# Kernel tuning notes

Hardware: AMD Instinct MI355X
Metric: run time of the kernel (lower is better)

## Reference

```python
import jax, jax.numpy as jnp
import numpy as np

D = 768
HEAD_SIZE = 64  # D / num_heads = 768 / 12

def setup_inputs() -> dict:
    key = jax.random.key(0)
    k1, k2, k3, k4 = jax.random.split(key, 4)
    ix = jax.random.normal(k1, (8, 4096, D), dtype=jnp.float32)
    # Linear(D, head_size, bias=False) weights; stored as [D, head_size] for x @ W
    scale = 1.0 / np.sqrt(D)
    Wk = jax.random.uniform(k2, (D, HEAD_SIZE), dtype=jnp.float32, minval=-scale, maxval=scale)
    Wq = jax.random.uniform(k3, (D, HEAD_SIZE), dtype=jnp.float32, minval=-scale, maxval=scale)
    Wv = jax.random.uniform(k4, (D, HEAD_SIZE), dtype=jnp.float32, minval=-scale, maxval=scale)
    return {"ix": ix, "Wk": Wk, "Wq": Wq, "Wv": Wv}

def reference(ix, Wk, Wq, Wv):
    # ix: [B, S, D]
    k = ix @ Wk  # [B, S, H]
    q = ix @ Wq  # [B, S, H]
    v = ix @ Wv  # [B, S, H]
    scale = 1.0 / jnp.sqrt(jnp.asarray(HEAD_SIZE, ix.dtype))
    wei = jnp.einsum('bsh,bth->bst', q, k) * scale  # [B, S, S]
    wei = jax.nn.softmax(wei, axis=-1)
    out = jnp.einsum('bst,bth->bsh', wei, v)  # [B, S, H]
    return out
```

## Files before the change

kernel.cpp:

```cpp
#include <hip/hip_runtime.h>
#include <hip/hip_bf16.h>

#define D_DIM 768
#define HS 64
#define SEQ 4096
#define NBATCH 8

typedef short bf8 __attribute__((ext_vector_type(8)));
typedef short bf4 __attribute__((ext_vector_type(4)));
typedef float f4 __attribute__((ext_vector_type(4)));

static __device__ __forceinline__ short f2b(float x) {
    __hip_bfloat16 h = __float2bfloat16(x);
    return __builtin_bit_cast(short, h);
}
static __device__ __forceinline__ unsigned pk2(float x, float y) {
    unsigned ux = __builtin_bit_cast(unsigned, x) + 0x8000u;
    unsigned uy = __builtin_bit_cast(unsigned, y) + 0x8000u;
    return __builtin_amdgcn_perm(uy, ux, 0x07060302u);
}

#if defined(__has_builtin)
#if __has_builtin(__builtin_amdgcn_exp2f)
#define EXP2F(x) __builtin_amdgcn_exp2f(x)
#endif
#endif
#ifndef EXP2F
#define EXP2F(x) exp2f(x)
#endif

__global__ __launch_bounds__(256) void wconv_kernel(
    const float* __restrict__ Wk, const float* __restrict__ Wq,
    const float* __restrict__ Wv, short* __restrict__ wt3)
{
    int tid = blockIdx.x * 256 + threadIdx.x;
    int mat = tid / (D_DIM * HS);
    int rem = tid - mat * (D_DIM * HS);
    int k = rem >> 6;
    int n = rem & 63;
    const float* W = (mat == 0) ? Wk : (mat == 1) ? Wq : Wv;
    float scale = (mat == 1) ? 0.18033688011112042f : 1.0f;
    int cc = mat * HS + n;
    int c = k >> 5, q = (k >> 3) & 3, e = k & 7;
    wt3[(c * 192 + cc) * 32 + q * 8 + e] = f2b(W[rem] * scale);
}

__global__ __launch_bounds__(256, 3) void proj_kernel(
    const float* __restrict__ ix, const short* __restrict__ wt3,
    short* __restrict__ qg, short* __restrict__ kg, short* __restrict__ vg)
{
    __shared__ short ixl[2][32 * 72];

    const int t = threadIdx.x;
    const int wave = t >> 6, lane = t & 63;
    const int m = lane & 15, quad = lane >> 4;
    const int m0 = blockIdx.x * 32;

    const int srow = t >> 3;
    const int skoff = (t & 7) * 8;

    f4 xr0, xr1;
    auto load_ix = [&](int c) {
        const float* px = ix + (m0 + srow) * D_DIM + c * 64 + skoff;
        xr0 = *(const f4*)px;
        xr1 = *(const f4*)(px + 4);
    };
    auto write_ix = [&](int p) {
        bf8 xw;
        #pragma unroll
        for (int i = 0; i < 4; ++i) { xw[i] = f2b(xr0[i]); xw[i + 4] = f2b(xr1[i]); }
        *(bf8*)(&ixl[p][srow * 72 + skoff]) = xw;
    };

    const int colb = wave * 48;
    const short* wbase = wt3 + (colb + m) * 32 + quad * 8;

    bf8 wb[2][2][3];
    auto load_w = [&](int c, int buf) {
        #pragma unroll
        for (int nt = 0; nt < 3; ++nt) {
            const short* pw = wbase + ((size_t)(2 * c) * 192 + nt * 16) * 32;
            wb[buf][0][nt] = *(const bf8*)pw;
            wb[buf][1][nt] = *(const bf8*)(pw + 192 * 32);
        }
    };

    f4 acc[2][3] = {};

    load_ix(0); load_w(0, 0); write_ix(0); __syncthreads();

    #pragma unroll
    for (int c = 0; c < 12; ++c) {
        const int p = c & 1;
        if (c + 1 < 12) { load_ix(c + 1); load_w(c + 1, (c + 1) & 1); }

        bf8 a0 = *(const bf8*)(&ixl[p][m * 72 + quad * 8]);
        bf8 a1 = *(const bf8*)(&ixl[p][m * 72 + 32 + quad * 8]);
        bf8 a2 = *(const bf8*)(&ixl[p][(16 + m) * 72 + quad * 8]);
        bf8 a3 = *(const bf8*)(&ixl[p][(16 + m) * 72 + 32 + quad * 8]);

        #pragma unroll
        for (int nt = 0; nt < 3; ++nt) {
            acc[0][nt] = __builtin_amdgcn_mfma_f32_16x16x32_bf16(a0, wb[p][0][nt], acc[0][nt], 0, 0, 0);
            acc[0][nt] = __builtin_amdgcn_mfma_f32_16x16x32_bf16(a1, wb[p][1][nt], acc[0][nt], 0, 0, 0);
            acc[1][nt] = __builtin_amdgcn_mfma_f32_16x16x32_bf16(a2, wb[p][0][nt], acc[1][nt], 0, 0, 0);
            acc[1][nt] = __builtin_amdgcn_mfma_f32_16x16x32_bf16(a3, wb[p][1][nt], acc[1][nt], 0, 0, 0);
        }

        if (c + 1 < 12) { write_ix((c + 1) & 1); __syncthreads(); }
    }

    #pragma unroll
    for (int mt = 0; mt < 2; ++mt) {
        const int row = m0 + mt * 16 + quad * 4;
        #pragma unroll
        for (int nt = 0; nt < 3; ++nt) {
            const int cb = colb + nt * 16;
            short* op = (cb < 64) ? kg : (cb < 128) ? qg : vg;
            const int n = (cb & 63) + m;
            #pragma unroll
            for (int r = 0; r < 4; ++r)
                op[(row + r) * HS + n] = f2b(acc[mt][nt][r]);
        }
    }
}

__global__ __launch_bounds__(256, 2) void attn_kernel(
    const short* __restrict__ qg, const short* __restrict__ kg,
    const short* __restrict__ vg, float* __restrict__ num0,
    float* __restrict__ num1, float* __restrict__ num2,
    float* __restrict__ num3, float* __restrict__ den0,
    float* __restrict__ den1, float* __restrict__ den2,
    float* __restrict__ den3)
{
    __shared__ short kl[2][64 * 72];
    __shared__ short vl[2][64 * 64];

    const int t = threadIdx.x;
    const int wave = t >> 6, lane = t & 63;
    const int m = lane & 15, quad = lane >> 4;

    const int flat = blockIdx.x;
    const int lg = (flat & 7) * 64 + (flat >> 3);
    const int qx = lg & 15;
    const int ks = (lg >> 4) & 3;
    const int b  = lg >> 6;

    const int rbase = b * SEQ;
    const int kbase = rbase + ks * (SEQ / 4);
    const int qw = qx * 256 + wave * 64;

    float* __restrict__ nump = (ks == 0) ? num0 : (ks == 1) ? num1 : (ks == 2) ? num2 : num3;
    float* __restrict__ denp = (ks == 0) ? den0 : (ks == 1) ? den1 : (ks == 2) ? den2 : den3;

    bf8 qf[4][2];
    #pragma unroll
    for (int nq = 0; nq < 4; ++nq)
        #pragma unroll
        for (int st = 0; st < 2; ++st)
            qf[nq][st] = *(const bf8*)(qg + (rbase + qw + nq * 16 + m) * HS + st * 32 + quad * 8);

    const int srow = t >> 2, soff = (t & 3) * 16;
    const int jp = t >> 3, dg = t & 7;
    const int j0 = jp * 2;
    const int jj = j0 & 31;
    const int gj = j0 >> 5;
    const int vq = (jj >> 2) & 3;
    const int vh = (jj >> 4) & 1;
    const int vb = (jj & 3) >> 1;
    const int vcol_base = vh * 4 + 2 * vb;
    const int vchunk_l = 4 * gj + vq;

    uint4 kr0, kr1, vr0, vr1;
    auto load_chunk = [&](int c) {
        const short* pk = kg + (kbase + c * 64 + srow) * HS + soff;
        kr0 = *(const uint4*)pk; kr1 = *(const uint4*)(pk + 8);
        const short* pv = vg + (kbase + c * 64 + j0) * HS + dg * 8;
        vr0 = *(const uint4*)pv; vr1 = *(const uint4*)(pv + HS);
    };
    auto write_chunk = [&](int p) {
        *(bf8*)(&kl[p][srow * 72 + soff])     = __builtin_bit_cast(bf8, kr0);
        *(bf8*)(&kl[p][srow * 72 + soff + 8]) = __builtin_bit_cast(bf8, kr1);
        bf8 v0 = __builtin_bit_cast(bf8, vr0), v1 = __builtin_bit_cast(bf8, vr1);
        #pragma unroll
        for (int i = 0; i < 8; ++i) {
            const int d = dg * 8 + i;
            const int chunk = vchunk_l ^ (i ^ dg);
            unsigned val = (unsigned short)v0[i] | ((unsigned)(unsigned short)v1[i] << 16);
            *(unsigned*)(&vl[p][d * 64 + chunk * 8 + vcol_base]) = val;
        }
    };

    f4 o[4][4] = {};
    float den[4] = {0.f, 0.f, 0.f, 0.f};

    load_chunk(0); write_chunk(0); __syncthreads();

    const int NCH = SEQ / 4 / 64;
    for (int c = 0; c < NCH; ++c) {
        const int p = c & 1;
        if (c + 1 < NCH) load_chunk(c + 1);

        #pragma unroll
        for (int g = 0; g < 2; ++g) {
            bf8 kA0 = *(const bf8*)(&kl[p][(g * 32 + m) * 72 + quad * 8]);
            bf8 kA1 = *(const bf8*)(&kl[p][(g * 32 + m) * 72 + 32 + quad * 8]);
            bf8 kB0 = *(const bf8*)(&kl[p][(g * 32 + 16 + m) * 72 + quad * 8]);
            bf8 kB1 = *(const bf8*)(&kl[p][(g * 32 + 16 + m) * 72 + 32 + quad * 8]);

            bf8 vf[4];
            #pragma unroll
            for (int dt = 0; dt < 4; ++dt) {
                const int row = dt * 16 + m;
                const int key = (m & 7) ^ (2 * dt + (m >> 3));
                const int chunk = (g * 4 + quad) ^ key;
                vf[dt] = *(const bf8*)(&vl[p][row * 64 + chunk * 8]);
            }

            #pragma unroll
            for (int nq = 0; nq < 4; ++nq) {
                f4 sa = {0.f, 0.f, 0.f, 0.f}, sb = {0.f, 0.f, 0.f, 0.f};
                sa = __builtin_amdgcn_mfma_f32_16x16x32_bf16(kA0, qf[nq][0], sa, 0, 0, 0);
                sa = __builtin_amdgcn_mfma_f32_16x16x32_bf16(kA1, qf[nq][1], sa, 0, 0, 0);
                sb = __builtin_amdgcn_mfma_f32_16x16x32_bf16(kB0, qf[nq][0], sb, 0, 0, 0);
                sb = __builtin_amdgcn_mfma_f32_16x16x32_bf16(kB1, qf[nq][1], sb, 0, 0, 0);
                float e0 = EXP2F(sa[0]), e1 = EXP2F(sa[1]), e2 = EXP2F(sa[2]), e3 = EXP2F(sa[3]);
                float e4 = EXP2F(sb[0]), e5 = EXP2F(sb[1]), e6 = EXP2F(sb[2]), e7 = EXP2F(sb[3]);
                den[nq] += ((e0 + e1) + (e2 + e3)) + ((e4 + e5) + (e6 + e7));
                uint4 pu;
                pu.x = pk2(e0, e1); pu.y = pk2(e2, e3);
                pu.z = pk2(e4, e5); pu.w = pk2(e6, e7);
                bf8 pf = __builtin_bit_cast(bf8, pu);
                #pragma unroll
                for (int dt = 0; dt < 4; ++dt)
                    o[nq][dt] = __builtin_amdgcn_mfma_f32_16x16x32_bf16(vf[dt], pf, o[nq][dt], 0, 0, 0);
            }
        }

        if (c + 1 < NCH) { write_chunk((c + 1) & 1); __syncthreads(); }
    }

    #pragma unroll
    for (int nq = 0; nq < 4; ++nq) {
        float d = den[nq];
        d += __shfl_xor(d, 16, 64);
        d += __shfl_xor(d, 32, 64);
        const int orow = rbase + qw + nq * 16 + m;
        if (quad == 0) denp[orow] = d;
        #pragma unroll
        for (int dt = 0; dt < 4; ++dt)
            *(f4*)(nump + orow * HS + dt * 16 + quad * 4) = o[nq][dt];
    }
}

__global__ __launch_bounds__(256) void reduce_kernel(
    float* __restrict__ out, const float* __restrict__ num1,
    const float* __restrict__ num2, const float* __restrict__ num3,
    const float* __restrict__ den0, const float* __restrict__ den1,
    const float* __restrict__ den2, const float* __restrict__ den3)
{
    const int gid = blockIdx.x * 256 + threadIdx.x;
    const int base = gid * 4;
    const int r = base >> 6;
    f4 n0 = *(const f4*)(out + base);
    f4 n1 = *(const f4*)(num1 + base);
    f4 n2 = *(const f4*)(num2 + base);
    f4 n3 = *(const f4*)(num3 + base);
    const float rs = 1.0f / ((den0[r] + den1[r]) + (den2[r] + den3[r]));
    f4 res;
    #pragma unroll
    for (int i = 0; i < 4; ++i) res[i] = ((n0[i] + n1[i]) + (n2[i] + n3[i])) * rs;
    *(f4*)(out + base) = res;
}

extern "C" void kernel_launch(void* const* d_in, const int* in_sizes, int n_in,
                              void* d_out, int out_size, void* d_ws, size_t ws_size,
                              hipStream_t stream) {
    const float* ix = (const float*)d_in[0];
    const float* Wk = (const float*)d_in[1];
    const float* Wq = (const float*)d_in[2];
    const float* Wv = (const float*)d_in[3];
    float* out = (float*)d_out;

    const size_t NQKV = (size_t)NBATCH * SEQ * HS;
    short* qg = (short*)d_ws;
    short* kg = qg + NQKV;
    short* vg = kg + NQKV;
    short* wt3 = vg + NQKV;
    char*  fbase = (char*)(wt3 + 24 * 192 * 32);
    float* num1 = (float*)fbase;
    float* num2 = num1 + NQKV;
    float* num3 = num2 + NQKV;
    float* den0 = num3 + NQKV;
    float* den1 = den0 + (size_t)NBATCH * SEQ;
    float* den2 = den1 + (size_t)NBATCH * SEQ;
    float* den3 = den2 + (size_t)NBATCH * SEQ;

    wconv_kernel<<<(3 * D_DIM * HS) / 256, 256, 0, stream>>>(Wk, Wq, Wv, wt3);
    proj_kernel<<<(NBATCH * SEQ) / 32, 256, 0, stream>>>(ix, wt3, qg, kg, vg);
    attn_kernel<<<512, 256, 0, stream>>>(qg, kg, vg, out, num1, num2, num3,
                                         den0, den1, den2, den3);
    reduce_kernel<<<(int)(NQKV / (256 * 4)), 256, 0, stream>>>(
        out, num1, num2, num3, den0, den1, den2, den3);
}
```

Measured before the change: 216.8 us.

## Load K fragments straight from global into registers, restage V, raise proj occupancy

The attention kernel no longer stages K through shared memory. Each wave loads its K MFMA fragments directly from global memory into double-buffered register sets, and the V staging is rewritten to use 4-row ushort4 loads with a new swizzled LDS write. Both kernels' loops are manually unrolled by two so the register buffers can ping-pong, and proj_kernel's launch bounds go from 3 to 4 blocks per CU. This is meant to cut LDS traffic and LDS footprint in attention. In exchange, each wave issues redundant global K loads and register pressure rises, which could cause spills at the higher proj occupancy.

Result: slower. 341.6 us (+57.5%).

```diff
diff --git a/kernel.cpp b/kernel.cpp
--- a/kernel.cpp
+++ b/kernel.cpp
@@ -45,7 +45,7 @@
     wt3[(c * 192 + cc) * 32 + q * 8 + e] = f2b(W[rem] * scale);
 }
 
-__global__ __launch_bounds__(256, 3) void proj_kernel(
+__global__ __launch_bounds__(256, 4) void proj_kernel(
     const float* __restrict__ ix, const short* __restrict__ wt3,
     short* __restrict__ qg, short* __restrict__ kg, short* __restrict__ vg)
 {
@@ -75,39 +75,42 @@
     const int colb = wave * 48;
     const short* wbase = wt3 + (colb + m) * 32 + quad * 8;
 
-    bf8 wb[2][2][3];
-    auto load_w = [&](int c, int buf) {
+    bf8 wbA[2][3], wbB[2][3];
+    auto load_w = [&](int c, bf8 (&dst)[2][3]) {
         #pragma unroll
         for (int nt = 0; nt < 3; ++nt) {
             const short* pw = wbase + ((size_t)(2 * c) * 192 + nt * 16) * 32;
-            wb[buf][0][nt] = *(const bf8*)pw;
-            wb[buf][1][nt] = *(const bf8*)(pw + 192 * 32);
+            dst[0][nt] = *(const bf8*)pw;
+            dst[1][nt] = *(const bf8*)(pw + 192 * 32);
         }
     };
 
     f4 acc[2][3] = {};
 
-    load_ix(0); load_w(0, 0); write_ix(0); __syncthreads();
-
-    #pragma unroll
-    for (int c = 0; c < 12; ++c) {
-        const int p = c & 1;
-        if (c + 1 < 12) { load_ix(c + 1); load_w(c + 1, (c + 1) & 1); }
-
+    auto compute = [&](const bf8 (&wb)[2][3], int p) {
         bf8 a0 = *(const bf8*)(&ixl[p][m * 72 + quad * 8]);
         bf8 a1 = *(const bf8*)(&ixl[p][m * 72 + 32 + quad * 8]);
         bf8 a2 = *(const bf8*)(&ixl[p][(16 + m) * 72 + quad * 8]);
         bf8 a3 = *(const bf8*)(&ixl[p][(16 + m) * 72 + 32 + quad * 8]);
-
         #pragma unroll
         for (int nt = 0; nt < 3; ++nt) {
-            acc[0][nt] = __builtin_amdgcn_mfma_f32_16x16x32_bf16(a0, wb[p][0][nt], acc[0][nt], 0, 0, 0);
-            acc[0][nt] = __builtin_amdgcn_mfma_f32_16x16x32_bf16(a1, wb[p][1][nt], acc[0][nt], 0, 0, 0);
-            acc[1][nt] = __builtin_amdgcn_mfma_f32_16x16x32_bf16(a2, wb[p][0][nt], acc[1][nt], 0, 0, 0);
-            acc[1][nt] = __builtin_amdgcn_mfma_f32_16x16x32_bf16(a3, wb[p][1][nt], acc[1][nt], 0, 0, 0);
-        }
-
-        if (c + 1 < 12) { write_ix((c + 1) & 1); __syncthreads(); }
+            acc[0][nt] = __builtin_amdgcn_mfma_f32_16x16x32_bf16(a0, wb[0][nt], acc[0][nt], 0, 0, 0);
+            acc[0][nt] = __builtin_amdgcn_mfma_f32_16x16x32_bf16(a1, wb[1][nt], acc[0][nt], 0, 0, 0);
+            acc[1][nt] = __builtin_amdgcn_mfma_f32_16x16x32_bf16(a2, wb[0][nt], acc[1][nt], 0, 0, 0);
+            acc[1][nt] = __builtin_amdgcn_mfma_f32_16x16x32_bf16(a3, wb[1][nt], acc[1][nt], 0, 0, 0);
+        }
+    };
+
+    load_ix(0); load_w(0, wbA); write_ix(0); __syncthreads();
+
+    for (int cc = 0; cc < 6; ++cc) {
+        const int c0 = 2 * cc, c1 = c0 + 1;
+        load_ix(c1); load_w(c1, wbB);
+        compute(wbA, 0);
+        write_ix(1); __syncthreads();
+        if (cc < 5) { load_ix(c0 + 2); load_w(c0 + 2, wbA); }
+        compute(wbB, 1);
+        if (cc < 5) { write_ix(0); __syncthreads(); }
     }
 
     #pragma unroll
@@ -133,7 +136,6 @@
     float* __restrict__ den1, float* __restrict__ den2,
     float* __restrict__ den3)
 {
-    __shared__ short kl[2][64 * 72];
     __shared__ short vl[2][64 * 64];
 
     const int t = threadIdx.x;
@@ -160,54 +162,49 @@
         for (int st = 0; st < 2; ++st)
             qf[nq][st] = *(const bf8*)(qg + (rbase + qw + nq * 16 + m) * HS + st * 32 + quad * 8);
 
-    const int srow = t >> 2, soff = (t & 3) * 16;
-    const int jp = t >> 3, dg = t & 7;
-    const int j0 = jp * 2;
-    const int jj = j0 & 31;
-    const int gj = j0 >> 5;
-    const int vq = (jj >> 2) & 3;
-    const int vh = (jj >> 4) & 1;
-    const int vb = (jj & 3) >> 1;
-    const int vcol_base = vh * 4 + 2 * vb;
-    const int vchunk_l = 4 * gj + vq;
-
-    uint4 kr0, kr1, vr0, vr1;
-    auto load_chunk = [&](int c) {
-        const short* pk = kg + (kbase + c * 64 + srow) * HS + soff;
-        kr0 = *(const uint4*)pk; kr1 = *(const uint4*)(pk + 8);
-        const short* pv = vg + (kbase + c * 64 + j0) * HS + dg * 8;
-        vr0 = *(const uint4*)pv; vr1 = *(const uint4*)(pv + HS);
-    };
-    auto write_chunk = [&](int p) {
-        *(bf8*)(&kl[p][srow * 72 + soff])     = __builtin_bit_cast(bf8, kr0);
-        *(bf8*)(&kl[p][srow * 72 + soff + 8]) = __builtin_bit_cast(bf8, kr1);
-        bf8 v0 = __builtin_bit_cast(bf8, vr0), v1 = __builtin_bit_cast(bf8, vr1);
-        #pragma unroll
-        for (int i = 0; i < 8; ++i) {
-            const int d = dg * 8 + i;
-            const int chunk = vchunk_l ^ (i ^ dg);
-            unsigned val = (unsigned short)v0[i] | ((unsigned)(unsigned short)v1[i] << 16);
-            *(unsigned*)(&vl[p][d * 64 + chunk * 8 + vcol_base]) = val;
+    const int jq = t >> 4, dq = t & 15;
+    const int vgj = jq >> 3, vh = (jq >> 2) & 1, vq = jq & 3;
+    const int vchunk_l = 4 * vgj + vq;
+    const int vcol = vh * 4;
+
+    ushort4 vr[4];
+    auto load_v = [&](int c) {
+        const short* pv = vg + (size_t)(kbase + c * 64 + jq * 4) * HS + dq * 4;
+        #pragma unroll
+        for (int r = 0; r < 4; ++r) vr[r] = *(const ushort4*)(pv + r * HS);
+    };
+    auto write_v = [&](int p) {
+        #pragma unroll
+        for (int i = 0; i < 4; ++i) {
+            const int d = dq * 4 + i;
+            const int chunk = vchunk_l ^ ((d & 7) ^ (d >> 3));
+            unsigned short e0 = (i == 0) ? vr[0].x : (i == 1) ? vr[0].y : (i == 2) ? vr[0].z : vr[0].w;
+            unsigned short e1 = (i == 0) ? vr[1].x : (i == 1) ? vr[1].y : (i == 2) ? vr[1].z : vr[1].w;
+            unsigned short e2 = (i == 0) ? vr[2].x : (i == 1) ? vr[2].y : (i == 2) ? vr[2].z : vr[2].w;
+            unsigned short e3 = (i == 0) ? vr[3].x : (i == 1) ? vr[3].y : (i == 2) ? vr[3].z : vr[3].w;
+            ushort4 w; w.x = e0; w.y = e1; w.z = e2; w.w = e3;
+            *(ushort4*)(&vl[p][d * 64 + chunk * 8 + vcol]) = w;
+        }
+    };
+
+    bf8 kfA[2][4], kfB[2][4];
+    auto load_k = [&](int c, bf8 (&dst)[2][4]) {
+        #pragma unroll
+        for (int g = 0; g < 2; ++g) {
+            const short* pk = kg + (size_t)(kbase + c * 64 + g * 32 + m) * HS + quad * 8;
+            dst[g][0] = *(const bf8*)pk;
+            dst[g][1] = *(const bf8*)(pk + 32);
+            dst[g][2] = *(const bf8*)(pk + 16 * HS);
+            dst[g][3] = *(const bf8*)(pk + 16 * HS + 32);
         }
     };
 
     f4 o[4][4] = {};
     float den[4] = {0.f, 0.f, 0.f, 0.f};
 
-    load_chunk(0); write_chunk(0); __syncthreads();
-
-    const int NCH = SEQ / 4 / 64;
-    for (int c = 0; c < NCH; ++c) {
-        const int p = c & 1;
-        if (c + 1 < NCH) load_chunk(c + 1);
-
+    auto compute = [&](const bf8 (&kc)[2][4], int p) {
         #pragma unroll
         for (int g = 0; g < 2; ++g) {
-            bf8 kA0 = *(const bf8*)(&kl[p][(g * 32 + m) * 72 + quad * 8]);
-            bf8 kA1 = *(const bf8*)(&kl[p][(g * 32 + m) * 72 + 32 + quad * 8]);
-            bf8 kB0 = *(const bf8*)(&kl[p][(g * 32 + 16 + m) * 72 + quad * 8]);
-            bf8 kB1 = *(const bf8*)(&kl[p][(g * 32 + 16 + m) * 72 + 32 + quad * 8]);
-
             bf8 vf[4];
             #pragma unroll
             for (int dt = 0; dt < 4; ++dt) {
@@ -216,14 +213,13 @@
                 const int chunk = (g * 4 + quad) ^ key;
                 vf[dt] = *(const bf8*)(&vl[p][row * 64 + chunk * 8]);
             }
-
             #pragma unroll
             for (int nq = 0; nq < 4; ++nq) {
                 f4 sa = {0.f, 0.f, 0.f, 0.f}, sb = {0.f, 0.f, 0.f, 0.f};
-                sa = __builtin_amdgcn_mfma_f32_16x16x32_bf16(kA0, qf[nq][0], sa, 0, 0, 0);
-                sa = __builtin_amdgcn_mfma_f32_16x16x32_bf16(kA1, qf[nq][1], sa, 0, 0, 0);
-                sb = __builtin_amdgcn_mfma_f32_16x16x32_bf16(kB0, qf[nq][0], sb, 0, 0, 0);
-                sb = __builtin_amdgcn_mfma_f32_16x16x32_bf16(kB1, qf[nq][1], sb, 0, 0, 0);
+                sa = __builtin_amdgcn_mfma_f32_16x16x32_bf16(kc[g][0], qf[nq][0], sa, 0, 0, 0);
+                sa = __builtin_amdgcn_mfma_f32_16x16x32_bf16(kc[g][1], qf[nq][1], sa, 0, 0, 0);
+                sb = __builtin_amdgcn_mfma_f32_16x16x32_bf16(kc[g][2], qf[nq][0], sb, 0, 0, 0);
+                sb = __builtin_amdgcn_mfma_f32_16x16x32_bf16(kc[g][3], qf[nq][1], sb, 0, 0, 0);
                 float e0 = EXP2F(sa[0]), e1 = EXP2F(sa[1]), e2 = EXP2F(sa[2]), e3 = EXP2F(sa[3]);
                 float e4 = EXP2F(sb[0]), e5 = EXP2F(sb[1]), e6 = EXP2F(sb[2]), e7 = EXP2F(sb[3]);
                 den[nq] += ((e0 + e1) + (e2 + e3)) + ((e4 + e5) + (e6 + e7));
@@ -236,8 +232,19 @@
                     o[nq][dt] = __builtin_amdgcn_mfma_f32_16x16x32_bf16(vf[dt], pf, o[nq][dt], 0, 0, 0);
             }
         }
-
-        if (c + 1 < NCH) { write_chunk((c + 1) & 1); __syncthreads(); }
+    };
+
+    load_v(0); load_k(0, kfA); write_v(0); __syncthreads();
+
+    const int NCH = SEQ / 4 / 64;
+    for (int cc = 0; cc < NCH / 2; ++cc) {
+        const int c0 = 2 * cc, c1 = c0 + 1;
+        load_v(c1); load_k(c1, kfB);
+        compute(kfA, 0);
+        write_v(1); __syncthreads();
+        if (cc < NCH / 2 - 1) { load_v(c0 + 2); load_k(c0 + 2, kfA); }
+        compute(kfB, 1);
+        if (cc < NCH / 2 - 1) { write_v(0); __syncthreads(); }
     }
 
     #pragma unroll
```
